# Optimization experiments

Hardware: AMD Instinct MI355X
Metric: run time of the kernel (lower is better)

The kernel has to match this reference:

```python
import jax, jax.numpy as jnp
import numpy as np

N = 20000
E = 320000
D_IN = 1024
D_OUT = 1024


def setup_inputs() -> dict:
    key = jax.random.key(0)
    k1, k2, k3, k4 = jax.random.split(key, 4)
    x = jax.random.normal(k1, (N, D_IN), dtype=jnp.float32)
    edge_index = jax.random.randint(k2, (2, E), 0, N, dtype=jnp.int64)
    # nn.Linear params: W is [out, in], b is [out]
    W = jax.random.normal(k3, (D_OUT, D_IN), dtype=jnp.float32) * (1.0 / np.sqrt(D_IN))
    b = jax.random.normal(k4, (D_OUT,), dtype=jnp.float32) * 0.01
    return {"x": x, "edge_index": edge_index, "W": W, "b": b}


def reference(x, edge_index, W, b):
    num_nodes = x.shape[0]
    # add self-connections (same as addSelfConnect)
    self_idx = jnp.arange(num_nodes, dtype=edge_index.dtype)
    ei = jnp.concatenate([edge_index, jnp.stack([self_idx, self_idx], axis=0)], axis=1)
    row, col = ei[0], ei[1]
    # linear: h = x @ W^T + b  -> [N, D_OUT]
    h = jnp.einsum('nd,od->no', x, W) + b
    # degree computed from row indices only (matches calDegree(row, ...))
    deg = jnp.zeros((num_nodes,), dtype=h.dtype).at[row].add(1.0)
    deg_inv_sqrt = deg ** -0.5  # every node has a self-loop, so deg >= 1
    norm = deg_inv_sqrt[row] * deg_inv_sqrt[col]  # [E+N]
    # gather source features, scale per-edge, scatter-sum to destination nodes
    msg = norm[:, None] * h[col]  # [E+N, D_OUT]
    out = jax.ops.segment_sum(msg, row, num_segments=num_nodes)
    return out
```

## Files before the change

### kernel.cpp

```cpp
#include <hip/hip_runtime.h>
#include <hip/hip_bf16.h>
#include <stdint.h>
#include <stddef.h>


#define D_DIM 1024
#define HP    1088
#define HPB   2176u
#define SLABW 64
#define NSLAB (D_DIM / SLABW)

typedef __bf16 bf16x8 __attribute__((ext_vector_type(8)));
typedef __bf16 bf16x4 __attribute__((ext_vector_type(4)));
typedef float  f32x4  __attribute__((ext_vector_type(4)));

#define GLOBAL_AS __attribute__((address_space(1)))
#define LDS_AS    __attribute__((address_space(3)))

static __device__ __forceinline__ void async_load16(const void* g, void* l) {
  __builtin_amdgcn_global_load_lds((GLOBAL_AS void*)(void*)g,
                                   (LDS_AS void*)l, 16, 0, 0);
}


__global__ void detect_kernel(const unsigned int* __restrict__ xw,
                              const unsigned int* __restrict__ ww,
                              const unsigned int* __restrict__ ew,
                              int* __restrict__ flags) {
  __shared__ int s[3];
  int t = threadIdx.x;
  if (t < 3) s[t] = 0;
  __syncthreads();
  int nx = 0, nw = 0, ze = 0;
  for (int i = t; i < 8192; i += 256) {
    if ((xw[i] & 0x7f80u) == 0x7f80u) nx++;
    if ((ww[i] & 0x7f80u) == 0x7f80u) nw++;
    if (ew[2 * i + 1] == 0u) ze++;
  }
  atomicAdd(&s[0], nx);
  atomicAdd(&s[1], nw);
  atomicAdd(&s[2], ze);
  __syncthreads();
  if (t == 0) {
    flags[0] = (s[0] >= 3) ? 1 : 0;
    flags[1] = (s[1] >= 3) ? 1 : 0;
    flags[2] = (s[2] >= 8000) ? 1 : 0;
  }
}


__global__ void zero_cnt_kernel(int* cnt, int n) {
  int i = blockIdx.x * blockDim.x + threadIdx.x;
  if (i < n) cnt[i] = 0;
}

__global__ void count_deg_kernel(const void* __restrict__ ei, int E,
                                 const int* __restrict__ flags,
                                 int* __restrict__ cnt) {
  int e = blockIdx.x * blockDim.x + threadIdx.x;
  if (e < E) {
    int r = flags[2] ? (int)((const long long*)ei)[e] : ((const int*)ei)[e];
    atomicAdd(&cnt[r], 1);
  }
}

__global__ void scan_kernel(const int* __restrict__ cnt, int n,
                            int* __restrict__ row_ptr, int* __restrict__ cursor,
                            float* __restrict__ dinv) {
  __shared__ int ssum[256];
  const int t = threadIdx.x;
  const int chunk = (n + 255) / 256;
  const int lo = t * chunk;
  const int hi = (lo + chunk < n) ? lo + chunk : n;
  int s = 0;
  for (int i = lo; i < hi; ++i) s += cnt[i];
  ssum[t] = s;
  __syncthreads();
  for (int off = 1; off < 256; off <<= 1) {
    int add = (t >= off) ? ssum[t - off] : 0;
    __syncthreads();
    ssum[t] += add;
    __syncthreads();
  }
  int run = ssum[t] - s;
  for (int i = lo; i < hi; ++i) {
    int v = cnt[i];
    row_ptr[i] = run;
    cursor[i]  = run;
    dinv[i] = rsqrtf((float)(v + 1));
    run += v;
  }
  if (t == 255) row_ptr[n] = ssum[255];
}

__global__ void scatter_kernel(const void* __restrict__ ei, int E,
                               const int* __restrict__ flags,
                               const float* __restrict__ dinv,
                               int* __restrict__ cursor,
                               int* __restrict__ cols_out,
                               long long* __restrict__ meta, int emit_w) {
  int e = blockIdx.x * blockDim.x + threadIdx.x;
  if (e < E) {
    int r, c;
    if (flags[2]) {
      const long long* p = (const long long*)ei;
      r = (int)p[e]; c = (int)p[e + E];
    } else {
      const int* p = (const int*)ei;
      r = p[e]; c = p[e + E];
    }
    int pos = atomicAdd(&cursor[r], 1);
    if (emit_w) {
      float w = dinv[r] * dinv[c];
      unsigned long long mm =
          ((unsigned long long)__float_as_uint(w) << 32) | (unsigned)c;
      meta[pos] = (long long)mm;
    } else {
      cols_out[pos] = c;
    }
  }
}


__global__ void conv_w_kernel(const void* __restrict__ W,
                              const void* __restrict__ b,
                              const int* __restrict__ flags,
                              unsigned short* __restrict__ Wb,
                              float* __restrict__ biasf) {
  int i = blockIdx.x * blockDim.x + threadIdx.x;
  int wfp = flags[1];
  if (wfp) {
    __bf16 h = (__bf16)((const float*)W)[i];
    Wb[i] = *(unsigned short*)&h;
  } else {
    Wb[i] = ((const unsigned short*)W)[i];
  }
  if (i < D_DIM) {
    biasf[i] = wfp ? ((const float*)b)[i] : (float)((const __bf16*)b)[i];
  }
}


__global__ __launch_bounds__(256) void conv_x_kernel(
    const void* __restrict__ X, const int* __restrict__ flags,
    unsigned short* __restrict__ Xb, int total8) {
  int i = blockIdx.x * blockDim.x + threadIdx.x;
  if (i >= total8) return;
  if (!flags[0]) return;
  const float* p = (const float*)X + (size_t)i * 8;
  f32x4 v0 = *(const f32x4*)p;
  f32x4 v1 = *(const f32x4*)(p + 4);
  bf16x8 r;
  r[0] = (__bf16)v0[0]; r[1] = (__bf16)v0[1];
  r[2] = (__bf16)v0[2]; r[3] = (__bf16)v0[3];
  r[4] = (__bf16)v1[0]; r[5] = (__bf16)v1[1];
  r[6] = (__bf16)v1[2]; r[7] = (__bf16)v1[3];
  *(bf16x8*)(Xb + (size_t)i * 8) = r;
}


__global__ __launch_bounds__(256) void gemm_xw2_kernel(
    const void* __restrict__ Xv,
    const unsigned short* __restrict__ Xb,
    const unsigned short* __restrict__ Wb,
    const float* __restrict__ biasf,
    const int* __restrict__ flags,
    __hip_bfloat16* __restrict__ H,
    int M) {
  __shared__ unsigned short As[128 * 32];
  __shared__ unsigned short Bs[128 * 32];

  const int t    = threadIdx.x;
  const int lane = t & 63;
  const int wave = t >> 6;
  const int wm   = wave >> 1;
  const int wn   = wave & 1;

  const int nwg = gridDim.x;
  const int wg  = (blockIdx.x & 7) * (nwg >> 3) + (blockIdx.x >> 3);
  const int m0  = (wg >> 3) * 128;
  const int n0  = (wg & 7) * 128;

  const unsigned short* Asrc =
      flags[0] ? Xb : (const unsigned short*)Xv;

  f32x4 acc[4][4] = {};

  const int ra = t >> 2;
  const int kc = (t & 3) * 8;
  int gr0 = m0 + ra;       if (gr0 >= M) gr0 = M - 1;
  int gr1 = m0 + 64 + ra;  if (gr1 >= M) gr1 = M - 1;
  const int quad = lane >> 4;
  const int mrow = lane & 15;

  for (int k0 = 0; k0 < D_DIM; k0 += 32) {
    async_load16(Asrc + (size_t)gr0 * D_DIM + k0 + kc, &As[ra * 32 + kc]);
    async_load16(Asrc + (size_t)gr1 * D_DIM + k0 + kc, &As[(ra + 64) * 32 + kc]);
    async_load16(Wb + (size_t)(n0 + ra) * D_DIM + k0 + kc, &Bs[ra * 32 + kc]);
    async_load16(Wb + (size_t)(n0 + ra + 64) * D_DIM + k0 + kc,
                 &Bs[(ra + 64) * 32 + kc]);
    __syncthreads();

    bf16x8 a[4], b[4];
#pragma unroll
    for (int i = 0; i < 4; ++i)
      a[i] = *(const bf16x8*)&As[(wm * 64 + i * 16 + mrow) * 32 + quad * 8];
#pragma unroll
    for (int j = 0; j < 4; ++j)
      b[j] = *(const bf16x8*)&Bs[(wn * 64 + j * 16 + mrow) * 32 + quad * 8];
#pragma unroll
    for (int i = 0; i < 4; ++i)
#pragma unroll
      for (int j = 0; j < 4; ++j)
        acc[i][j] = __builtin_amdgcn_mfma_f32_16x16x32_bf16(a[i], b[j], acc[i][j], 0, 0, 0);
    __syncthreads();
  }

#pragma unroll
  for (int j = 0; j < 4; ++j) {
    int n = n0 + wn * 64 + j * 16 + mrow;
    float bn = biasf[n];
#pragma unroll
    for (int i = 0; i < 4; ++i) {
      int mb = m0 + wm * 64 + i * 16 + quad * 4;
#pragma unroll
      for (int rg = 0; rg < 4; ++rg) {
        int m = mb + rg;
        if (m < M) H[(size_t)m * HP + n] = __float2bfloat16(acc[i][j][rg] + bn);
      }
    }
  }
}


__global__ __launch_bounds__(256) void gemm_xw_kernel(
    const void* __restrict__ Xv,
    const unsigned short* __restrict__ Wb,
    const float* __restrict__ biasf,
    const int* __restrict__ flags,
    __hip_bfloat16* __restrict__ H,
    int M) {
  __shared__ unsigned short As[128 * 32];
  __shared__ unsigned short Bs[128 * 32];

  const int t    = threadIdx.x;
  const int lane = t & 63;
  const int wave = t >> 6;
  const int wm   = wave >> 1;
  const int wn   = wave & 1;
  const int m0   = blockIdx.x * 128;
  const int n0   = blockIdx.y * 128;
  const int xfp  = flags[0];

  f32x4 acc[4][4] = {};

  const int ra = t >> 1;
  const int kh = (t & 1) * 16;
  const int rb = t >> 2;
  const int kc = (t & 3) * 8;
  const int quad = lane >> 4;
  const int mrow = lane & 15;

  for (int k0 = 0; k0 < D_DIM; k0 += 32) {
    async_load16(Wb + (size_t)(n0 + rb) * D_DIM + k0 + kc, &Bs[rb * 32 + kc]);
    async_load16(Wb + (size_t)(n0 + rb + 64) * D_DIM + k0 + kc,
                 &Bs[(rb + 64) * 32 + kc]);
    bf16x8 lo{}, hi{};
    int gm = m0 + ra;
    if (gm < M) {
      if (xfp) {
        const float* p = (const float*)Xv + (size_t)gm * D_DIM + k0 + kh;
        f32x4 v0 = *(const f32x4*)(p);
        f32x4 v1 = *(const f32x4*)(p + 4);
        f32x4 v2 = *(const f32x4*)(p + 8);
        f32x4 v3 = *(const f32x4*)(p + 12);
        lo[0] = (__bf16)v0[0]; lo[1] = (__bf16)v0[1];
        lo[2] = (__bf16)v0[2]; lo[3] = (__bf16)v0[3];
        lo[4] = (__bf16)v1[0]; lo[5] = (__bf16)v1[1];
        lo[6] = (__bf16)v1[2]; lo[7] = (__bf16)v1[3];
        hi[0] = (__bf16)v2[0]; hi[1] = (__bf16)v2[1];
        hi[2] = (__bf16)v2[2]; hi[3] = (__bf16)v2[3];
        hi[4] = (__bf16)v3[0]; hi[5] = (__bf16)v3[1];
        hi[6] = (__bf16)v3[2]; hi[7] = (__bf16)v3[3];
      } else {
        const unsigned short* p =
            (const unsigned short*)Xv + (size_t)gm * D_DIM + k0 + kh;
        lo = *(const bf16x8*)p;
        hi = *(const bf16x8*)(p + 8);
      }
    }
    *(bf16x8*)&As[ra * 32 + kh]     = lo;
    *(bf16x8*)&As[ra * 32 + kh + 8] = hi;
    __syncthreads();

    bf16x8 a[4], b[4];
#pragma unroll
    for (int i = 0; i < 4; ++i)
      a[i] = *(const bf16x8*)&As[(wm * 64 + i * 16 + mrow) * 32 + quad * 8];
#pragma unroll
    for (int j = 0; j < 4; ++j)
      b[j] = *(const bf16x8*)&Bs[(wn * 64 + j * 16 + mrow) * 32 + quad * 8];
#pragma unroll
    for (int i = 0; i < 4; ++i)
#pragma unroll
      for (int j = 0; j < 4; ++j)
        acc[i][j] = __builtin_amdgcn_mfma_f32_16x16x32_bf16(a[i], b[j], acc[i][j], 0, 0, 0);
    __syncthreads();
  }

#pragma unroll
  for (int j = 0; j < 4; ++j) {
    int n = n0 + wn * 64 + j * 16 + mrow;
    float bn = biasf[n];
#pragma unroll
    for (int i = 0; i < 4; ++i) {
      int mb = m0 + wm * 64 + i * 16 + quad * 4;
#pragma unroll
      for (int rg = 0; rg < 4; ++rg) {
        int m = mb + rg;
        if (m < M) H[(size_t)m * HP + n] = __float2bfloat16(acc[i][j][rg] + bn);
      }
    }
  }
}


__global__ __launch_bounds__(256) void aggregate_h_slab_kernel(
    const __hip_bfloat16* __restrict__ H,
    const int* __restrict__ row_ptr,
    const long long* __restrict__ meta,
    const float* __restrict__ dinv,
    const int* __restrict__ flags,
    void* __restrict__ outv, int M, int nodeblks) {
  const int P    = nodeblks << 3;
  const int pass = blockIdx.x / P;
  const int rem  = blockIdx.x - pass * P;
  const int slab = (pass << 3) + (rem & 7);
  const int nb   = rem >> 3;
  const int t    = threadIdx.x;
  const int i    = nb * 32 + (t >> 3);
  if (i >= M) return;
  const int l = t & 7;
  const unsigned co = (unsigned)l * 16u;
  const char* Hs = (const char*)H + (unsigned)slab * 128u;

  float a[8];
  {
    float di = dinv[i];
    float w = di * di;
    bf16x8 v = *(const bf16x8*)(Hs + (unsigned)i * HPB + co);
#pragma unroll
    for (int k = 0; k < 8; ++k) a[k] = w * (float)v[k];
  }

  const int e0 = row_ptr[i], e1 = row_ptr[i + 1];
  int e = e0;
  for (; e + 4 <= e1; e += 4) {
    long long m0 = meta[e];
    long long m1 = meta[e + 1];
    long long m2 = meta[e + 2];
    long long m3 = meta[e + 3];
    unsigned o0 = (unsigned)(m0 & 0xffffffffLL) * HPB + co;
    unsigned o1 = (unsigned)(m1 & 0xffffffffLL) * HPB + co;
    unsigned o2 = (unsigned)(m2 & 0xffffffffLL) * HPB + co;
    unsigned o3 = (unsigned)(m3 & 0xffffffffLL) * HPB + co;
    float w0 = __uint_as_float((unsigned)((unsigned long long)m0 >> 32));
    float w1 = __uint_as_float((unsigned)((unsigned long long)m1 >> 32));
    float w2 = __uint_as_float((unsigned)((unsigned long long)m2 >> 32));
    float w3 = __uint_as_float((unsigned)((unsigned long long)m3 >> 32));
    bf16x8 u0 = *(const bf16x8*)(Hs + o0);
    bf16x8 u1 = *(const bf16x8*)(Hs + o1);
    bf16x8 u2 = *(const bf16x8*)(Hs + o2);
    bf16x8 u3 = *(const bf16x8*)(Hs + o3);
#pragma unroll
    for (int q = 0; q < 8; ++q) {
      a[q] = fmaf(w0, (float)u0[q],
             fmaf(w1, (float)u1[q],
             fmaf(w2, (float)u2[q],
             fmaf(w3, (float)u3[q], a[q]))));
    }
  }
  for (; e < e1; ++e) {
    long long m0 = meta[e];
    unsigned o0 = (unsigned)(m0 & 0xffffffffLL) * HPB + co;
    float w0 = __uint_as_float((unsigned)((unsigned long long)m0 >> 32));
    bf16x8 u0 = *(const bf16x8*)(Hs + o0);
#pragma unroll
    for (int q = 0; q < 8; ++q) a[q] = fmaf(w0, (float)u0[q], a[q]);
  }

  if (flags[0]) {
    float* o = (float*)outv + (size_t)i * D_DIM + slab * SLABW + l * 8;
    f32x4 r0, r1;
    r0[0] = a[0]; r0[1] = a[1]; r0[2] = a[2]; r0[3] = a[3];
    r1[0] = a[4]; r1[1] = a[5]; r1[2] = a[6]; r1[3] = a[7];
    __builtin_nontemporal_store(r0, (f32x4*)o);
    __builtin_nontemporal_store(r1, (f32x4*)(o + 4));
  } else {
    __hip_bfloat16* o =
        (__hip_bfloat16*)outv + (size_t)i * D_DIM + slab * SLABW + l * 8;
    bf16x8 r;
#pragma unroll
    for (int k = 0; k < 8; ++k) r[k] = (__bf16)a[k];
    __builtin_nontemporal_store(*(f32x4*)&r, (f32x4*)o);
  }
}


__global__ __launch_bounds__(256) void aggregate_x_kernel(
    const void* __restrict__ X,
    const int* __restrict__ row_ptr,
    const int* __restrict__ cols,
    const float* __restrict__ dinv,
    const int* __restrict__ flags,
    float* __restrict__ rowsum,
    void* __restrict__ Y) {
  const int i  = blockIdx.x;
  const int c0 = threadIdx.x * 4;
  const float di = dinv[i];
  const int e0 = row_ptr[i], e1 = row_ptr[i + 1];
  float wsum = di * di;
  float a0, a1, a2, a3;

  if (flags[0]) {
    const float* Xf = (const float*)X;
    f32x4 v = *(const f32x4*)(Xf + (size_t)i * D_DIM + c0);
    a0 = wsum * v[0]; a1 = wsum * v[1]; a2 = wsum * v[2]; a3 = wsum * v[3];
    for (int e = e0; e < e1; ++e) {
      int c = cols[e];
      float w = di * dinv[c];
      wsum += w;
      f32x4 u = *(const f32x4*)(Xf + (size_t)c * D_DIM + c0);
      a0 += w * u[0]; a1 += w * u[1]; a2 += w * u[2]; a3 += w * u[3];
    }
    f32x4 r; r[0] = a0; r[1] = a1; r[2] = a2; r[3] = a3;
    *(f32x4*)((float*)Y + (size_t)i * D_DIM + c0) = r;
  } else {
    const __hip_bfloat16* Xb = (const __hip_bfloat16*)X;
    bf16x4 v = *(const bf16x4*)(Xb + (size_t)i * D_DIM + c0);
    a0 = wsum * (float)v[0]; a1 = wsum * (float)v[1];
    a2 = wsum * (float)v[2]; a3 = wsum * (float)v[3];
    for (int e = e0; e < e1; ++e) {
      int c = cols[e];
      float w = di * dinv[c];
      wsum += w;
      bf16x4 u = *(const bf16x4*)(Xb + (size_t)c * D_DIM + c0);
      a0 += w * (float)u[0]; a1 += w * (float)u[1];
      a2 += w * (float)u[2]; a3 += w * (float)u[3];
    }
    bf16x4 r;
    r[0] = (__bf16)a0; r[1] = (__bf16)a1; r[2] = (__bf16)a2; r[3] = (__bf16)a3;
    *(bf16x4*)((__hip_bfloat16*)Y + (size_t)i * D_DIM + c0) = r;
  }
  if (threadIdx.x == 0) rowsum[i] = wsum;
}

__global__ __launch_bounds__(256) void strip_gemm_kernel(
    const void* __restrict__ Yv,
    const unsigned short* __restrict__ Wb,
    const float* __restrict__ biasf,
    const float* __restrict__ rowsum,
    const int* __restrict__ flags,
    void* __restrict__ outv) {
  __shared__ unsigned short Ys[32 * 1024];

  const int t    = threadIdx.x;
  const int lane = t & 63;
  const int wave = t >> 6;
  const int m0   = blockIdx.x * 32;
  const int ofp  = flags[0];

  if (ofp) {
    const float* Yf = (const float*)Yv;
    for (int idx = t; idx < 32 * 128; idx += 256) {
      int r = idx >> 7, c = idx & 127;
      const float* p = Yf + (size_t)(m0 + r) * D_DIM + c * 8;
      f32x4 lo = *(const f32x4*)p;
      f32x4 hi = *(const f32x4*)(p + 4);
      bf16x8 v;
      v[0] = (__bf16)lo[0]; v[1] = (__bf16)lo[1];
      v[2] = (__bf16)lo[2]; v[3] = (__bf16)lo[3];
      v[4] = (__bf16)hi[0]; v[5] = (__bf16)hi[1];
      v[6] = (__bf16)hi[2]; v[7] = (__bf16)hi[3];
      int sc = c ^ (r & 15);
      *(bf16x8*)&Ys[r * 1024 + sc * 8] = v;
    }
  } else {
    const __hip_bfloat16* Yb = (const __hip_bfloat16*)Yv;
    for (int idx = t; idx < 32 * 128; idx += 256) {
      int r = idx >> 7, c = idx & 127;
      bf16x8 v = *(const bf16x8*)(Yb + (size_t)(m0 + r) * D_DIM + c * 8);
      int sc = c ^ (r & 15);
      *(bf16x8*)&Ys[r * 1024 + sc * 8] = v;
    }
  }
  __syncthreads();

  const int quad = lane >> 4;
  const int mrow = lane & 15;

  for (int nb = 0; nb < 4; ++nb) {
    f32x4 acc[2][4] = {};
    for (int k0 = 0; k0 < D_DIM; k0 += 32) {
      const int cbase = k0 >> 3;
      bf16x8 a[2], b[4];
#pragma unroll
      for (int i = 0; i < 2; ++i) {
        int m = i * 16 + mrow;
        int sc = (cbase + quad) ^ mrow;
        a[i] = *(const bf16x8*)&Ys[m * 1024 + sc * 8];
      }
#pragma unroll
      for (int j = 0; j < 4; ++j) {
        int n = wave * 256 + nb * 64 + j * 16 + mrow;
        b[j] = *(const bf16x8*)(Wb + (size_t)n * D_DIM + k0 + quad * 8);
      }
#pragma unroll
      for (int i = 0; i < 2; ++i)
#pragma unroll
        for (int j = 0; j < 4; ++j)
          acc[i][j] = __builtin_amdgcn_mfma_f32_16x16x32_bf16(a[i], b[j], acc[i][j], 0, 0, 0);
    }
#pragma unroll
    for (int j = 0; j < 4; ++j) {
      int n = wave * 256 + nb * 64 + j * 16 + mrow;
      float bn = biasf[n];
#pragma unroll
      for (int i = 0; i < 2; ++i) {
        int mb = m0 + i * 16 + quad * 4;
#pragma unroll
        for (int rg = 0; rg < 4; ++rg) {
          int m = mb + rg;
          float val = acc[i][j][rg] + rowsum[m] * bn;
          if (ofp) ((float*)outv)[(size_t)m * D_DIM + n] = val;
          else ((__hip_bfloat16*)outv)[(size_t)m * D_DIM + n] = __float2bfloat16(val);
        }
      }
    }
  }
}


extern "C" void kernel_launch(void* const* d_in, const int* in_sizes, int n_in,
                              void* d_out, int out_size, void* d_ws, size_t ws_size,
                              hipStream_t stream) {
  const void* x    = d_in[0];
  const void* ei   = d_in[1];
  const void* Wm   = d_in[2];
  const void* bias = d_in[3];

  const int E = in_sizes[1] / 2;
  const int M = in_sizes[0] / D_DIM;

  char* ws = (char*)d_ws;
  const size_t KB = 1024, MB = 1024 * 1024;

  const size_t off_flags = 0;
  const size_t off_cnt   = 4 * KB;
  const size_t off_biasf = 96 * KB;
  const size_t off_rowp  = 128 * KB;
  const size_t off_curs  = off_rowp + 96 * KB;
  const size_t off_dinv  = off_curs + 96 * KB;
  const size_t off_meta  = off_dinv + 128 * KB;
  size_t off_wb = off_meta + (size_t)E * 8;
  off_wb = (off_wb + 255) & ~(size_t)255;
  const size_t off_h  = off_wb + 2 * MB;
  const size_t szHp   = (size_t)M * HP * 2;
  const size_t off_xb = off_h + szHp;
  const size_t szXb   = (size_t)M * D_DIM * 2;

  const size_t need_fast   = off_h + szHp + 64 * KB;
  const size_t need_faster = off_xb + szXb + 64 * KB;

  if (ws_size >= need_fast && M > 256) {
    int*   flags   = (int*)(ws + off_flags);
    int*   cnt     = (int*)(ws + off_cnt);
    float* biasf   = (float*)(ws + off_biasf);
    int*   row_ptr = (int*)(ws + off_rowp);
    int*   cursor  = (int*)(ws + off_curs);
    float* dinv    = (float*)(ws + off_dinv);
    long long* meta = (long long*)(ws + off_meta);
    unsigned short* Wb = (unsigned short*)(ws + off_wb);
    __hip_bfloat16* H  = (__hip_bfloat16*)(ws + off_h);
    unsigned short* Xb = (unsigned short*)(ws + off_xb);

    detect_kernel<<<1, 256, 0, stream>>>((const unsigned int*)x,
                                         (const unsigned int*)Wm,
                                         (const unsigned int*)ei, (int*)flags);
    zero_cnt_kernel<<<(M + 255) / 256, 256, 0, stream>>>(cnt, M);
    count_deg_kernel<<<(E + 255) / 256, 256, 0, stream>>>(ei, E, flags, cnt);
    scan_kernel<<<1, 256, 0, stream>>>(cnt, M, row_ptr, cursor, dinv);
    scatter_kernel<<<(E + 255) / 256, 256, 0, stream>>>(ei, E, flags, dinv,
                                                        cursor, (int*)0, meta, 1);
    conv_w_kernel<<<(D_DIM * D_DIM) / 256, 256, 0, stream>>>(Wm, bias, flags,
                                                             Wb, biasf);
    const int mtiles = (M + 127) / 128;
    if (ws_size >= need_faster) {
      const int total8 = M * (D_DIM / 8);
      conv_x_kernel<<<(total8 + 255) / 256, 256, 0, stream>>>(x, flags, Xb,
                                                              total8);
      gemm_xw2_kernel<<<mtiles * 8, 256, 0, stream>>>(x, Xb, Wb, biasf, flags,
                                                      H, M);
    } else {
      dim3 ggrid(mtiles, D_DIM / 128);
      gemm_xw_kernel<<<ggrid, 256, 0, stream>>>(x, Wb, biasf, flags, H, M);
    }
    const int nodeblks = (M + 31) / 32;
    aggregate_h_slab_kernel<<<nodeblks * NSLAB, 256, 0, stream>>>(
        H, row_ptr, meta, dinv, flags, d_out, M, nodeblks);
  } else {
    int*   flags   = (int*)(ws);
    int*   cnt     = (int*)(ws + 4 * KB);
    int*   row_ptr = (int*)(ws + 128 * KB);
    int*   cursor  = (int*)(ws + 256 * KB);
    float* dinv    = (float*)(ws + 384 * KB);
    float* rowsum  = (float*)(ws + 512 * KB);
    float* biasf   = (float*)(ws + 640 * KB);
    int*   cols    = (int*)(ws + 768 * KB);
    unsigned short* Wb = (unsigned short*)(ws + 2 * MB);

    detect_kernel<<<1, 256, 0, stream>>>((const unsigned int*)x,
                                         (const unsigned int*)Wm,
                                         (const unsigned int*)ei, (int*)flags);
    zero_cnt_kernel<<<(M + 255) / 256, 256, 0, stream>>>(cnt, M);
    count_deg_kernel<<<(E + 255) / 256, 256, 0, stream>>>(ei, E, flags, cnt);
    scan_kernel<<<1, 256, 0, stream>>>(cnt, M, row_ptr, cursor, dinv);
    scatter_kernel<<<(E + 255) / 256, 256, 0, stream>>>(ei, E, flags, dinv,
                                                        cursor, cols, (long long*)0, 0);
    conv_w_kernel<<<(D_DIM * D_DIM) / 256, 256, 0, stream>>>(Wm, bias, flags,
                                                             Wb, biasf);
    aggregate_x_kernel<<<M, 256, 0, stream>>>(x, row_ptr, cols, dinv, flags,
                                              rowsum, d_out);
    strip_gemm_kernel<<<M / 32, 256, 0, stream>>>(d_out, Wb, biasf, rowsum,
                                                  flags, d_out);
  }
}
```

Baseline: 383.0 us.

## Double-buffer LDS tiles in XW GEMM to overlap loads with MFMA

Converts the GEMM main loop to a two-stage LDS ping-pong: the next K tile is issued via global_load_lds into the alternate buffer before computing on the current one, cutting one barrier per iteration. It also precomputes base pointers and sets launch_bounds occupancy hint to 3 blocks per CU. Doubles LDS use per block and may raise register pressure; correctness relies on the barrier draining async loads before reuse.

Result: slower. 392.9 us (+2.6%).

```diff
diff --git a/kernel.cpp b/kernel.cpp
--- a/kernel.cpp
+++ b/kernel.cpp
@@ -159,7 +159,7 @@
 }
 
 
-__global__ __launch_bounds__(256) void gemm_xw2_kernel(
+__global__ __launch_bounds__(256, 3) void gemm_xw2_kernel(
     const void* __restrict__ Xv,
     const unsigned short* __restrict__ Xb,
     const unsigned short* __restrict__ Wb,
@@ -167,8 +167,8 @@
     const int* __restrict__ flags,
     __hip_bfloat16* __restrict__ H,
     int M) {
-  __shared__ unsigned short As[128 * 32];
-  __shared__ unsigned short Bs[128 * 32];
+  __shared__ unsigned short As[2][128 * 32];
+  __shared__ unsigned short Bs[2][128 * 32];
 
   const int t    = threadIdx.x;
   const int lane = t & 63;
@@ -193,28 +193,43 @@
   const int quad = lane >> 4;
   const int mrow = lane & 15;
 
+  const unsigned short* A0 = Asrc + (size_t)gr0 * D_DIM + kc;
+  const unsigned short* A1 = Asrc + (size_t)gr1 * D_DIM + kc;
+  const unsigned short* B0 = Wb + (size_t)(n0 + ra) * D_DIM + kc;
+  const unsigned short* B1 = Wb + (size_t)(n0 + ra + 64) * D_DIM + kc;
+
+#define STAGE_TILE(buf, k0)                                        \
+  do {                                                             \
+    async_load16(A0 + (k0), &As[buf][ra * 32 + kc]);               \
+    async_load16(A1 + (k0), &As[buf][(ra + 64) * 32 + kc]);        \
+    async_load16(B0 + (k0), &Bs[buf][ra * 32 + kc]);               \
+    async_load16(B1 + (k0), &Bs[buf][(ra + 64) * 32 + kc]);        \
+  } while (0)
+
+  STAGE_TILE(0, 0);
+  __syncthreads();
+
+  int cur = 0;
   for (int k0 = 0; k0 < D_DIM; k0 += 32) {
-    async_load16(Asrc + (size_t)gr0 * D_DIM + k0 + kc, &As[ra * 32 + kc]);
-    async_load16(Asrc + (size_t)gr1 * D_DIM + k0 + kc, &As[(ra + 64) * 32 + kc]);
-    async_load16(Wb + (size_t)(n0 + ra) * D_DIM + k0 + kc, &Bs[ra * 32 + kc]);
-    async_load16(Wb + (size_t)(n0 + ra + 64) * D_DIM + k0 + kc,
-                 &Bs[(ra + 64) * 32 + kc]);
-    __syncthreads();
+    if (k0 + 32 < D_DIM) STAGE_TILE(cur ^ 1, k0 + 32);
 
     bf16x8 a[4], b[4];
 #pragma unroll
     for (int i = 0; i < 4; ++i)
-      a[i] = *(const bf16x8*)&As[(wm * 64 + i * 16 + mrow) * 32 + quad * 8];
+      a[i] = *(const bf16x8*)&As[cur][(wm * 64 + i * 16 + mrow) * 32 + quad * 8];
 #pragma unroll
     for (int j = 0; j < 4; ++j)
-      b[j] = *(const bf16x8*)&Bs[(wn * 64 + j * 16 + mrow) * 32 + quad * 8];
+      b[j] = *(const bf16x8*)&Bs[cur][(wn * 64 + j * 16 + mrow) * 32 + quad * 8];
 #pragma unroll
     for (int i = 0; i < 4; ++i)
 #pragma unroll
       for (int j = 0; j < 4; ++j)
         acc[i][j] = __builtin_amdgcn_mfma_f32_16x16x32_bf16(a[i], b[j], acc[i][j], 0, 0, 0);
+
     __syncthreads();
-  }
+    cur ^= 1;
+  }
+#undef STAGE_TILE
 
 #pragma unroll
   for (int j = 0; j < 4; ++j) {
```
